# Kernel tuning notes

Hardware: AMD Instinct MI355X
Metric: run time of the kernel (lower is better)

The kernel has to match this reference:

```python
import jax, jax.numpy as jnp
import numpy as np

N_NODES = 100000
N_EDGES = 3200000
IN_CH = 128
HIDDEN = 128
N_CLASSES = 40


def setup_inputs() -> dict:
    key = jax.random.key(0)
    k1, k2, k3, k4 = jax.random.split(key, 4)
    x = jax.random.normal(k1, (N_NODES, IN_CH), dtype=jnp.float32)
    edge_index = jax.random.randint(k2, (2, N_EDGES), 0, N_NODES, dtype=jnp.int64)
    W1 = jax.random.normal(k3, (IN_CH, HIDDEN), dtype=jnp.float32) * (1.0 / np.sqrt(IN_CH))
    b1 = jnp.zeros((HIDDEN,), dtype=jnp.float32)
    W2 = jax.random.normal(k4, (HIDDEN, N_CLASSES), dtype=jnp.float32) * (1.0 / np.sqrt(HIDDEN))
    b2 = jnp.zeros((N_CLASSES,), dtype=jnp.float32)
    return {"x": x, "edge_index": edge_index, "W1": W1, "b1": b1, "W2": W2, "b2": b2}


def gcn_conv(x, src, dst, norm, W, b, n_nodes):
    # PyG GCNConv: h = x @ W; out[dst] += norm * h[src]; out += b
    h = x @ W
    msg = h[src] * norm[:, None]          # [E+N, F_out] gathered messages
    out = jax.ops.segment_sum(msg, dst, num_segments=n_nodes)
    return out + b


def reference(x, edge_index, W1, b1, W2, b2):
    n = x.shape[0]
    loop = jnp.arange(n, dtype=edge_index.dtype)
    src = jnp.concatenate([edge_index[0], loop])  # add self-loops (PyG default)
    dst = jnp.concatenate([edge_index[1], loop])
    w = jnp.ones(src.shape[0], dtype=x.dtype)
    deg = jax.ops.segment_sum(w, dst, num_segments=n)
    dinv = jnp.where(deg > 0, jax.lax.rsqrt(deg), 0.0)
    norm = dinv[src] * dinv[dst]  # symmetric normalization per edge

    h1 = jax.nn.relu(gcn_conv(x, src, dst, norm, W1, b1, n))
    # dropout is identity in eval mode
    out = gcn_conv(h1, src, dst, norm, W2, b2, n)
    return out
```

## Files before the change

kernel.cpp:

```cpp
#include <hip/hip_runtime.h>


static inline size_t align256(size_t x) { return (x + 255) & ~(size_t)255; }

#define BIN_CHUNK 16384
#define MAX_NB 511

__device__ __forceinline__ unsigned bf16pack2(float a, float b) {
  union { float f; unsigned u; } ua, ub;
  ua.f = a; ub.f = b;
  unsigned ra = (ua.u + 0x7fffu + ((ua.u >> 16) & 1u)) >> 16;
  unsigned rb = (ub.u + 0x7fffu + ((ub.u >> 16) & 1u)) >> 16;
  return ra | (rb << 16);
}

__device__ __forceinline__ void acc_bf16x8(float* acc, uint4 v) {
  union { unsigned u; float f; } c;
  c.u = v.x << 16;          acc[0] += c.f;
  c.u = v.x & 0xffff0000u;  acc[1] += c.f;
  c.u = v.y << 16;          acc[2] += c.f;
  c.u = v.y & 0xffff0000u;  acc[3] += c.f;
  c.u = v.z << 16;          acc[4] += c.f;
  c.u = v.z & 0xffff0000u;  acc[5] += c.f;
  c.u = v.w << 16;          acc[6] += c.f;
  c.u = v.w & 0xffff0000u;  acc[7] += c.f;
}

__global__ void zero_k(int* __restrict__ p, int n) {
  int i = blockIdx.x * blockDim.x + threadIdx.x;
  if (i < n) p[i] = 0;
}

__global__ __launch_bounds__(256) void bucket_count_k(const int* __restrict__ dst,
                                                      int* __restrict__ btot,
                                                      int E, int NB) {
  __shared__ int hist[MAX_NB];
  int t = threadIdx.x;
  for (int b = t; b < NB; b += 256) hist[b] = 0;
  __syncthreads();
  int e0 = blockIdx.x * BIN_CHUNK;
  int e1 = min(e0 + BIN_CHUNK, E);
  for (int e = e0 + t; e < e1; e += 256) atomicAdd(&hist[dst[e] >> 8], 1);
  __syncthreads();
  for (int b = t; b < NB; b += 256)
    if (hist[b]) atomicAdd(&btot[b], hist[b]);
}

__global__ __launch_bounds__(512) void bucket_scan_k(const int* __restrict__ btot,
                                                     int* __restrict__ base,
                                                     int* __restrict__ bcur,
                                                     int NB, int E) {
  __shared__ int ws[8];
  int t = threadIdx.x, lane = t & 63, w = t >> 6;
  int v = (t < NB) ? btot[t] : 0;
  int incl = v;
#pragma unroll
  for (int off = 1; off < 64; off <<= 1) {
    int u = __shfl_up(incl, off, 64);
    if (lane >= off) incl += u;
  }
  if (lane == 63) ws[w] = incl;
  __syncthreads();
  int woff = 0;
  for (int k = 0; k < w; ++k) woff += ws[k];
  int excl = woff + incl - v;
  if (t < NB) { base[t] = excl; bcur[t] = excl; }
  if (t == 0) base[NB] = E;
}

__global__ __launch_bounds__(256) void binpart_k(const int* __restrict__ src,
                                                 const int* __restrict__ dst,
                                                 int* __restrict__ bcur,
                                                 uint2* __restrict__ binned,
                                                 int E, int NB) {
  __shared__ int hist[MAX_NB];
  int t = threadIdx.x;
  int e0 = blockIdx.x * BIN_CHUNK;
  int e1 = min(e0 + BIN_CHUNK, E);
  for (int b = t; b < NB; b += 256) hist[b] = 0;
  __syncthreads();
  for (int e = e0 + t; e < e1; e += 256) atomicAdd(&hist[dst[e] >> 8], 1);
  __syncthreads();
  for (int b = t; b < NB; b += 256) {
    int h = hist[b];
    hist[b] = h ? atomicAdd(&bcur[b], h) : 0;
  }
  __syncthreads();
  for (int e = e0 + t; e < e1; e += 256) {
    int d = dst[e];
    int r = atomicAdd(&hist[d >> 8], 1);
    binned[r] = make_uint2((unsigned)src[e], (unsigned)d);
  }
}

__global__ __launch_bounds__(256) void binscat2_k(const uint2* __restrict__ binned,
                                                  const int* __restrict__ base,
                                                  int* __restrict__ counts,
                                                  int* __restrict__ rowoff,
                                                  float* __restrict__ dinv,
                                                  int* __restrict__ col, int N) {
  __shared__ int cnt[256];
  __shared__ int lcur[256];
  __shared__ int ws[4];
  int b = blockIdx.x, t = threadIdx.x;
  int lo = base[b], hi = base[b + 1];
  cnt[t] = 0;
  __syncthreads();
  for (int e = lo + t; e < hi; e += 256) atomicAdd(&cnt[binned[e].y & 255], 1);
  __syncthreads();
  int v = cnt[t];
  int lane = t & 63, w = t >> 6;
  int incl = v;
#pragma unroll
  for (int off = 1; off < 64; off <<= 1) {
    int u = __shfl_up(incl, off, 64);
    if (lane >= off) incl += u;
  }
  if (lane == 63) ws[w] = incl;
  __syncthreads();
  int woff = 0;
  for (int k = 0; k < w; ++k) woff += ws[k];
  int loff = woff + incl - v;
  int node = (b << 8) + t;
  if (node < N) {
    counts[node] = v;
    rowoff[node] = lo + loff;
    dinv[node] = rsqrtf((float)(v + 1));
  }
  lcur[t] = lo + loff;
  __syncthreads();
  for (int e = lo + t; e < hi; e += 256) {
    uint2 rec = binned[e];
    int p = atomicAdd(&lcur[rec.y & 255], 1);
    col[p] = (int)rec.x;
  }
}

__global__ __launch_bounds__(256) void gemm1_k(const float* __restrict__ x,
                                               const float* __restrict__ W,
                                               const float* __restrict__ dinv,
                                               unsigned* __restrict__ g1, int n) {
  __shared__ float Xs[64][68];
  __shared__ float Ws[64][132];
  int t = threadIdx.x;
  int row0 = blockIdx.x * 64;
  int cg = t & 15, rg = t >> 4;
  int c0 = cg * 8, r0 = rg * 4;

  float acc[4][8];
#pragma unroll
  for (int r = 0; r < 4; ++r)
#pragma unroll
    for (int c = 0; c < 8; ++c) acc[r][c] = 0.f;

  for (int ks = 0; ks < 2; ++ks) {
    __syncthreads();
#pragma unroll
    for (int q = 0; q < 4; ++q) {
      int f = t + q * 256;
      int r = f >> 4, c4 = f & 15;
      int grow = row0 + r;
      float4 v = make_float4(0.f, 0.f, 0.f, 0.f);
      if (grow < n) v = *(const float4*)(x + (size_t)grow * 128 + ks * 64 + c4 * 4);
      *(float4*)&Xs[r][c4 * 4] = v;
    }
#pragma unroll
    for (int q = 0; q < 8; ++q) {
      int f = t + q * 256;
      int k = f >> 5, c4 = f & 31;
      float4 v = *(const float4*)(W + (size_t)(ks * 64 + k) * 128 + c4 * 4);
      *(float4*)&Ws[k][c4 * 4] = v;
    }
    __syncthreads();

#pragma unroll
    for (int k4 = 0; k4 < 16; ++k4) {
      float4 xv0 = *(const float4*)&Xs[r0 + 0][k4 * 4];
      float4 xv1 = *(const float4*)&Xs[r0 + 1][k4 * 4];
      float4 xv2 = *(const float4*)&Xs[r0 + 2][k4 * 4];
      float4 xv3 = *(const float4*)&Xs[r0 + 3][k4 * 4];
#pragma unroll
      for (int kk = 0; kk < 4; ++kk) {
        const float* wrow = &Ws[k4 * 4 + kk][0];
        float4 wa = *(const float4*)(wrow + c0);
        float4 wb = *(const float4*)(wrow + c0 + 4);
        float a0 = kk == 0 ? xv0.x : kk == 1 ? xv0.y : kk == 2 ? xv0.z : xv0.w;
        float a1 = kk == 0 ? xv1.x : kk == 1 ? xv1.y : kk == 2 ? xv1.z : xv1.w;
        float a2 = kk == 0 ? xv2.x : kk == 1 ? xv2.y : kk == 2 ? xv2.z : xv2.w;
        float a3 = kk == 0 ? xv3.x : kk == 1 ? xv3.y : kk == 2 ? xv3.z : xv3.w;
        float as[4] = {a0, a1, a2, a3};
#pragma unroll
        for (int r = 0; r < 4; ++r) {
          acc[r][0] += as[r] * wa.x; acc[r][1] += as[r] * wa.y;
          acc[r][2] += as[r] * wa.z; acc[r][3] += as[r] * wa.w;
          acc[r][4] += as[r] * wb.x; acc[r][5] += as[r] * wb.y;
          acc[r][6] += as[r] * wb.z; acc[r][7] += as[r] * wb.w;
        }
      }
    }
  }

#pragma unroll
  for (int r = 0; r < 4; ++r) {
    int grow = row0 + r0 + r;
    if (grow < n) {
      float s = dinv[grow];
      uint4 pv;
      pv.x = bf16pack2(acc[r][0] * s, acc[r][1] * s);
      pv.y = bf16pack2(acc[r][2] * s, acc[r][3] * s);
      pv.z = bf16pack2(acc[r][4] * s, acc[r][5] * s);
      pv.w = bf16pack2(acc[r][6] * s, acc[r][7] * s);
      ((uint4*)g1)[(size_t)grow * 16 + cg] = pv;
    }
  }
}

__global__ __launch_bounds__(256) void agg1_k(const unsigned* __restrict__ g1,
                                              const int* __restrict__ col,
                                              const int* __restrict__ rowoff,
                                              const int* __restrict__ counts,
                                              const float* __restrict__ dinv,
                                              const float* __restrict__ b1,
                                              float* __restrict__ h1, int n) {
  int w = threadIdx.x >> 6, lane = threadIdx.x & 63;
  int i = blockIdx.x * 4 + w;
  if (i >= n) return;
  int q = lane >> 4, c8 = lane & 15;
  const uint4* g1v = (const uint4*)g1;
  int start = rowoff[i], cnt = counts[i];

  float acc[8] = {0.f, 0.f, 0.f, 0.f, 0.f, 0.f, 0.f, 0.f};
  if (q == 0) acc_bf16x8(acc, g1v[(size_t)i * 16 + c8]);

#pragma unroll 4
  for (int e = q; e < cnt; e += 4) {
    int j = col[start + e];
    acc_bf16x8(acc, g1v[(size_t)j * 16 + c8]);
  }

#pragma unroll
  for (int k = 0; k < 8; ++k) {
    acc[k] += __shfl_xor(acc[k], 16, 64);
    acc[k] += __shfl_xor(acc[k], 32, 64);
  }

  if (q == 0) {
    float di = dinv[i];
    float4 ba = *(const float4*)(b1 + c8 * 8);
    float4 bb = *(const float4*)(b1 + c8 * 8 + 4);
    float4 o0, o1;
    o0.x = fmaxf(di * acc[0] + ba.x, 0.f);
    o0.y = fmaxf(di * acc[1] + ba.y, 0.f);
    o0.z = fmaxf(di * acc[2] + ba.z, 0.f);
    o0.w = fmaxf(di * acc[3] + ba.w, 0.f);
    o1.x = fmaxf(di * acc[4] + bb.x, 0.f);
    o1.y = fmaxf(di * acc[5] + bb.y, 0.f);
    o1.z = fmaxf(di * acc[6] + bb.z, 0.f);
    o1.w = fmaxf(di * acc[7] + bb.w, 0.f);
    float* o = h1 + (size_t)i * 128 + c8 * 8;
    *(float4*)o = o0;
    *(float4*)(o + 4) = o1;
  }
}

__global__ __launch_bounds__(256) void gemm2_k(const float* __restrict__ h1,
                                               const float* __restrict__ W2,
                                               const float* __restrict__ dinv,
                                               unsigned* __restrict__ g2, int n) {
  __shared__ float Xs[64][68];
  __shared__ float Ws[64][68];
  int t = threadIdx.x;
  int row0 = blockIdx.x * 64;
  int cg = t & 7, rg = t >> 3;
  int c0 = cg * 8, r0 = rg * 2;

  float acc[2][8];
#pragma unroll
  for (int r = 0; r < 2; ++r)
#pragma unroll
    for (int c = 0; c < 8; ++c) acc[r][c] = 0.f;

  for (int idx = t; idx < 64 * 68; idx += 256) ((float*)Ws)[idx] = 0.f;

  for (int ks = 0; ks < 2; ++ks) {
    __syncthreads();
#pragma unroll
    for (int q = 0; q < 4; ++q) {
      int f = t + q * 256;
      int r = f >> 4, c4 = f & 15;
      int grow = row0 + r;
      float4 v = make_float4(0.f, 0.f, 0.f, 0.f);
      if (grow < n) v = *(const float4*)(h1 + (size_t)grow * 128 + ks * 64 + c4 * 4);
      *(float4*)&Xs[r][c4 * 4] = v;
    }
#pragma unroll
    for (int q = 0; q < 3; ++q) {
      int f = t + q * 256;
      if (f < 640) {
        int k = f / 10, c4 = f % 10;
        float4 v = *(const float4*)(W2 + (size_t)(ks * 64 + k) * 40 + c4 * 4);
        *(float4*)&Ws[k][c4 * 4] = v;
      }
    }
    __syncthreads();

#pragma unroll
    for (int k4 = 0; k4 < 16; ++k4) {
      float4 x0 = *(const float4*)&Xs[r0 + 0][k4 * 4];
      float4 x1 = *(const float4*)&Xs[r0 + 1][k4 * 4];
#pragma unroll
      for (int kk = 0; kk < 4; ++kk) {
        const float* wrow = &Ws[k4 * 4 + kk][0];
        float4 wa = *(const float4*)(wrow + c0);
        float4 wb = *(const float4*)(wrow + c0 + 4);
        float a0 = kk == 0 ? x0.x : kk == 1 ? x0.y : kk == 2 ? x0.z : x0.w;
        float a1 = kk == 0 ? x1.x : kk == 1 ? x1.y : kk == 2 ? x1.z : x1.w;
        acc[0][0] += a0 * wa.x; acc[0][1] += a0 * wa.y;
        acc[0][2] += a0 * wa.z; acc[0][3] += a0 * wa.w;
        acc[0][4] += a0 * wb.x; acc[0][5] += a0 * wb.y;
        acc[0][6] += a0 * wb.z; acc[0][7] += a0 * wb.w;
        acc[1][0] += a1 * wa.x; acc[1][1] += a1 * wa.y;
        acc[1][2] += a1 * wa.z; acc[1][3] += a1 * wa.w;
        acc[1][4] += a1 * wb.x; acc[1][5] += a1 * wb.y;
        acc[1][6] += a1 * wb.z; acc[1][7] += a1 * wb.w;
      }
    }
  }

#pragma unroll
  for (int r = 0; r < 2; ++r) {
    int grow = row0 + r0 + r;
    if (grow < n) {
      float s = dinv[grow];
      uint4 pv;
      pv.x = bf16pack2(acc[r][0] * s, acc[r][1] * s);
      pv.y = bf16pack2(acc[r][2] * s, acc[r][3] * s);
      pv.z = bf16pack2(acc[r][4] * s, acc[r][5] * s);
      pv.w = bf16pack2(acc[r][6] * s, acc[r][7] * s);
      ((uint4*)g2)[(size_t)grow * 8 + cg] = pv;
    }
  }
}

__global__ __launch_bounds__(256) void agg2_k(const unsigned* __restrict__ g2,
                                              const int* __restrict__ col,
                                              const int* __restrict__ rowoff,
                                              const int* __restrict__ counts,
                                              const float* __restrict__ dinv,
                                              const float* __restrict__ b2,
                                              float* __restrict__ out, int n) {
  int w = threadIdx.x >> 6, lane = threadIdx.x & 63;
  int i = blockIdx.x * 4 + w;
  if (i >= n) return;
  int q = lane >> 3, c8 = lane & 7;
  const uint4* g2v = (const uint4*)g2;
  int start = rowoff[i], cnt = counts[i];

  float acc[8] = {0.f, 0.f, 0.f, 0.f, 0.f, 0.f, 0.f, 0.f};
  if (q == 0) acc_bf16x8(acc, g2v[(size_t)i * 8 + c8]);

#pragma unroll 4
  for (int e = q; e < cnt; e += 8) {
    int j = col[start + e];
    acc_bf16x8(acc, g2v[(size_t)j * 8 + c8]);
  }

#pragma unroll
  for (int k = 0; k < 8; ++k) {
    acc[k] += __shfl_xor(acc[k], 8, 64);
    acc[k] += __shfl_xor(acc[k], 16, 64);
    acc[k] += __shfl_xor(acc[k], 32, 64);
  }

  if (lane < 5) {
    float di = dinv[i];
    float4 ba = *(const float4*)(b2 + lane * 8);
    float4 bb = *(const float4*)(b2 + lane * 8 + 4);
    float4 o0, o1;
    o0.x = di * acc[0] + ba.x;
    o0.y = di * acc[1] + ba.y;
    o0.z = di * acc[2] + ba.z;
    o0.w = di * acc[3] + ba.w;
    o1.x = di * acc[4] + bb.x;
    o1.y = di * acc[5] + bb.y;
    o1.z = di * acc[6] + bb.z;
    o1.w = di * acc[7] + bb.w;
    float* o = out + (size_t)i * 40 + lane * 8;
    *(float4*)o = o0;
    *(float4*)(o + 4) = o1;
  }
}

extern "C" void kernel_launch(void* const* d_in, const int* in_sizes, int n_in,
                              void* d_out, int out_size, void* d_ws, size_t ws_size,
                              hipStream_t stream) {
  const float* x  = (const float*)d_in[0];
  const int*   ei = (const int*)d_in[1];
  const float* W1 = (const float*)d_in[2];
  const float* b1 = (const float*)d_in[3];
  const float* W2 = (const float*)d_in[4];
  const float* b2 = (const float*)d_in[5];
  float* out = (float*)d_out;

  const int N = in_sizes[0] / 128;
  const int E = in_sizes[1] / 2;
  const int* src = ei;
  const int* dst = ei + E;
  const int NB = (N + 255) / 256;

  size_t off = 0;
  auto alloc = [&](size_t bytes) {
    char* p = (char*)d_ws + off;
    off = align256(off + bytes);
    return (void*)p;
  };
  int*      counts = (int*)alloc((size_t)N * 4);
  int*      rowoff = (int*)alloc((size_t)N * 4);
  float*    dinv   = (float*)alloc((size_t)N * 4);
  int*      btot   = (int*)alloc((size_t)NB * 4);
  int*      base   = (int*)alloc((size_t)(NB + 1) * 4);
  int*      bcur   = (int*)alloc((size_t)NB * 4);
  int*      col    = (int*)alloc((size_t)E * 4);
  uint2*    binned = (uint2*)alloc((size_t)E * 8);
  unsigned* g1     = (unsigned*)alloc((size_t)N * 128 * 2);
  float*    h1     = (float*)alloc((size_t)N * 128 * 4);
  unsigned* g2     = g1;
  if (off > ws_size) return;
  if (NB > MAX_NB) return;

  int gA = (N + 3) / 4;
  int gBin = (E + BIN_CHUNK - 1) / BIN_CHUNK;

  zero_k<<<(NB + 255) / 256, 256, 0, stream>>>(btot, NB);
  bucket_count_k<<<gBin, 256, 0, stream>>>(dst, btot, E, NB);
  bucket_scan_k<<<1, 512, 0, stream>>>(btot, base, bcur, NB, E);
  binpart_k<<<gBin, 256, 0, stream>>>(src, dst, bcur, binned, E, NB);
  binscat2_k<<<NB, 256, 0, stream>>>(binned, base, counts, rowoff, dinv, col, N);
  gemm1_k<<<(N + 63) / 64, 256, 0, stream>>>(x, W1, dinv, g1, N);
  agg1_k<<<gA, 256, 0, stream>>>(g1, col, rowoff, counts, dinv, b1, h1, N);
  gemm2_k<<<(N + 63) / 64, 256, 0, stream>>>(h1, W2, dinv, g2, N);
  agg2_k<<<gA, 256, 0, stream>>>(g2, col, rowoff, counts, dinv, b2, out, N);
}
```

Baseline: 505.7 us.

## Pack binned edge records into 32 bits and split aggregation by feature slices

The binned edge buffer now stores src<<8 | (dst&255) in one 32-bit word instead of a uint2 pair. This halves the traffic of the partition and scatter passes. The aggregation kernels now split the feature dimension into 32-channel slices handled by separate blocks. Each wave processes 16 edges in parallel per slice, with 4 lanes per 64-byte row chunk. This raises the number of edges in flight per row, but each neighbor's col index is reloaded once per slice and it adds more shuffle reductions. The src<<8 packing assumes node ids below 2^24.

```diff
diff --git a/kernel.cpp b/kernel.cpp
--- a/kernel.cpp
+++ b/kernel.cpp
@@ -71,7 +71,7 @@
 __global__ __launch_bounds__(256) void binpart_k(const int* __restrict__ src,
                                                  const int* __restrict__ dst,
                                                  int* __restrict__ bcur,
-                                                 uint2* __restrict__ binned,
+                                                 unsigned* __restrict__ binned,
                                                  int E, int NB) {
   __shared__ int hist[MAX_NB];
   int t = threadIdx.x;
@@ -89,11 +89,11 @@
   for (int e = e0 + t; e < e1; e += 256) {
     int d = dst[e];
     int r = atomicAdd(&hist[d >> 8], 1);
-    binned[r] = make_uint2((unsigned)src[e], (unsigned)d);
-  }
-}
-
-__global__ __launch_bounds__(256) void binscat2_k(const uint2* __restrict__ binned,
+    binned[r] = ((unsigned)src[e] << 8) | ((unsigned)d & 255u);
+  }
+}
+
+__global__ __launch_bounds__(256) void binscat2_k(const unsigned* __restrict__ binned,
                                                   const int* __restrict__ base,
                                                   int* __restrict__ counts,
                                                   int* __restrict__ rowoff,
@@ -106,7 +106,7 @@
   int lo = base[b], hi = base[b + 1];
   cnt[t] = 0;
   __syncthreads();
-  for (int e = lo + t; e < hi; e += 256) atomicAdd(&cnt[binned[e].y & 255], 1);
+  for (int e = lo + t; e < hi; e += 256) atomicAdd(&cnt[binned[e] & 255u], 1);
   __syncthreads();
   int v = cnt[t];
   int lane = t & 63, w = t >> 6;
@@ -130,9 +130,9 @@
   lcur[t] = lo + loff;
   __syncthreads();
   for (int e = lo + t; e < hi; e += 256) {
-    uint2 rec = binned[e];
-    int p = atomicAdd(&lcur[rec.y & 255], 1);
-    col[p] = (int)rec.x;
+    unsigned rec = binned[e];
+    int p = atomicAdd(&lcur[rec & 255u], 1);
+    col[p] = (int)(rec >> 8);
   }
 }
 
@@ -221,33 +221,39 @@
                                               const int* __restrict__ counts,
                                               const float* __restrict__ dinv,
                                               const float* __restrict__ b1,
-                                              float* __restrict__ h1, int n) {
+                                              float* __restrict__ h1, int n,
+                                              int NBA) {
   int w = threadIdx.x >> 6, lane = threadIdx.x & 63;
-  int i = blockIdx.x * 4 + w;
+  int p = blockIdx.x / NBA;
+  int i = (blockIdx.x % NBA) * 4 + w;
   if (i >= n) return;
-  int q = lane >> 4, c8 = lane & 15;
+  int q = lane >> 2, c = lane & 3;
   const uint4* g1v = (const uint4*)g1;
   int start = rowoff[i], cnt = counts[i];
+  int slice = p * 4 + c;
 
   float acc[8] = {0.f, 0.f, 0.f, 0.f, 0.f, 0.f, 0.f, 0.f};
-  if (q == 0) acc_bf16x8(acc, g1v[(size_t)i * 16 + c8]);
-
-#pragma unroll 4
-  for (int e = q; e < cnt; e += 4) {
+  if (q == 0) acc_bf16x8(acc, g1v[(size_t)i * 16 + slice]);
+
+#pragma unroll 2
+  for (int e = q; e < cnt; e += 16) {
     int j = col[start + e];
-    acc_bf16x8(acc, g1v[(size_t)j * 16 + c8]);
+    acc_bf16x8(acc, g1v[(size_t)j * 16 + slice]);
   }
 
 #pragma unroll
   for (int k = 0; k < 8; ++k) {
+    acc[k] += __shfl_xor(acc[k], 4, 64);
+    acc[k] += __shfl_xor(acc[k], 8, 64);
     acc[k] += __shfl_xor(acc[k], 16, 64);
     acc[k] += __shfl_xor(acc[k], 32, 64);
   }
 
   if (q == 0) {
     float di = dinv[i];
-    float4 ba = *(const float4*)(b1 + c8 * 8);
-    float4 bb = *(const float4*)(b1 + c8 * 8 + 4);
+    int ch = p * 32 + c * 8;
+    float4 ba = *(const float4*)(b1 + ch);
+    float4 bb = *(const float4*)(b1 + ch + 4);
     float4 o0, o1;
     o0.x = fmaxf(di * acc[0] + ba.x, 0.f);
     o0.y = fmaxf(di * acc[1] + ba.y, 0.f);
@@ -257,7 +263,7 @@
     o1.y = fmaxf(di * acc[5] + bb.y, 0.f);
     o1.z = fmaxf(di * acc[6] + bb.z, 0.f);
     o1.w = fmaxf(di * acc[7] + bb.w, 0.f);
-    float* o = h1 + (size_t)i * 128 + c8 * 8;
+    float* o = h1 + (size_t)i * 128 + ch;
     *(float4*)o = o0;
     *(float4*)(o + 4) = o1;
   }
@@ -348,34 +354,39 @@
                                               const int* __restrict__ counts,
                                               const float* __restrict__ dinv,
                                               const float* __restrict__ b2,
-                                              float* __restrict__ out, int n) {
+                                              float* __restrict__ out, int n,
+                                              int NBA) {
   int w = threadIdx.x >> 6, lane = threadIdx.x & 63;
-  int i = blockIdx.x * 4 + w;
+  int p = blockIdx.x / NBA;
+  int i = (blockIdx.x % NBA) * 4 + w;
   if (i >= n) return;
-  int q = lane >> 3, c8 = lane & 7;
+  int q = lane >> 2, c = lane & 3;
   const uint4* g2v = (const uint4*)g2;
   int start = rowoff[i], cnt = counts[i];
+  int slice = p * 4 + c;
 
   float acc[8] = {0.f, 0.f, 0.f, 0.f, 0.f, 0.f, 0.f, 0.f};
-  if (q == 0) acc_bf16x8(acc, g2v[(size_t)i * 8 + c8]);
-
-#pragma unroll 4
-  for (int e = q; e < cnt; e += 8) {
+  if (q == 0) acc_bf16x8(acc, g2v[(size_t)i * 8 + slice]);
+
+#pragma unroll 2
+  for (int e = q; e < cnt; e += 16) {
     int j = col[start + e];
-    acc_bf16x8(acc, g2v[(size_t)j * 8 + c8]);
+    acc_bf16x8(acc, g2v[(size_t)j * 8 + slice]);
   }
 
 #pragma unroll
   for (int k = 0; k < 8; ++k) {
+    acc[k] += __shfl_xor(acc[k], 4, 64);
     acc[k] += __shfl_xor(acc[k], 8, 64);
     acc[k] += __shfl_xor(acc[k], 16, 64);
     acc[k] += __shfl_xor(acc[k], 32, 64);
   }
 
-  if (lane < 5) {
+  int ch = p * 32 + c * 8;
+  if (q == 0 && ch < 40) {
     float di = dinv[i];
-    float4 ba = *(const float4*)(b2 + lane * 8);
-    float4 bb = *(const float4*)(b2 + lane * 8 + 4);
+    float4 ba = *(const float4*)(b2 + ch);
+    float4 bb = *(const float4*)(b2 + ch + 4);
     float4 o0, o1;
     o0.x = di * acc[0] + ba.x;
     o0.y = di * acc[1] + ba.y;
@@ -385,7 +396,7 @@
     o1.y = di * acc[5] + bb.y;
     o1.z = di * acc[6] + bb.z;
     o1.w = di * acc[7] + bb.w;
-    float* o = out + (size_t)i * 40 + lane * 8;
+    float* o = out + (size_t)i * 40 + ch;
     *(float4*)o = o0;
     *(float4*)(o + 4) = o1;
   }
@@ -421,14 +432,14 @@
   int*      base   = (int*)alloc((size_t)(NB + 1) * 4);
   int*      bcur   = (int*)alloc((size_t)NB * 4);
   int*      col    = (int*)alloc((size_t)E * 4);
-  uint2*    binned = (uint2*)alloc((size_t)E * 8);
+  unsigned* binned = (unsigned*)alloc((size_t)E * 4);
   unsigned* g1     = (unsigned*)alloc((size_t)N * 128 * 2);
   float*    h1     = (float*)alloc((size_t)N * 128 * 4);
   unsigned* g2     = g1;
   if (off > ws_size) return;
   if (NB > MAX_NB) return;
 
-  int gA = (N + 3) / 4;
+  const int NBA = (N + 3) / 4;
   int gBin = (E + BIN_CHUNK - 1) / BIN_CHUNK;
 
   zero_k<<<(NB + 255) / 256, 256, 0, stream>>>(btot, NB);
@@ -437,7 +448,7 @@
   binpart_k<<<gBin, 256, 0, stream>>>(src, dst, bcur, binned, E, NB);
   binscat2_k<<<NB, 256, 0, stream>>>(binned, base, counts, rowoff, dinv, col, N);
   gemm1_k<<<(N + 63) / 64, 256, 0, stream>>>(x, W1, dinv, g1, N);
-  agg1_k<<<gA, 256, 0, stream>>>(g1, col, rowoff, counts, dinv, b1, h1, N);
+  agg1_k<<<4 * NBA, 256, 0, stream>>>(g1, col, rowoff, counts, dinv, b1, h1, N, NBA);
   gemm2_k<<<(N + 63) / 64, 256, 0, stream>>>(h1, W2, dinv, g2, N);
-  agg2_k<<<gA, 256, 0, stream>>>(g2, col, rowoff, counts, dinv, b2, out, N);
-}
+  agg2_k<<<2 * NBA, 256, 0, stream>>>(g2, col, rowoff, counts, dinv, b2, out, N, NBA);
+}
```

Measured after the change: 620.6 us. +22.7%, slower.

## Use bf16 MFMA for first GEMM and pack binned edges into 32 bits

Applied to the files above, without the earlier changes.

The first-layer GEMM moves from scalar fp32 FMAs to bf16 MFMA 16x16x32 instructions. It uses a 128-row tile, converts inputs to bf16 in LDS, and stages the output through LDS for coalesced stores. Separately, each binned edge record is packed into one 32-bit word (src<<8 | dst&255) instead of a uint2, which halves the traffic of the binning pass. The bf16 rounding of x and W1 adds precision loss, and the packing assumes src fits in 24 bits.

```diff
diff --git a/kernel.cpp b/kernel.cpp
--- a/kernel.cpp
+++ b/kernel.cpp
@@ -5,6 +5,9 @@
 
 #define BIN_CHUNK 16384
 #define MAX_NB 511
+
+typedef float f32x4 __attribute__((ext_vector_type(4)));
+typedef short s16x8 __attribute__((ext_vector_type(8)));
 
 __device__ __forceinline__ unsigned bf16pack2(float a, float b) {
   union { float f; unsigned u; } ua, ub;
@@ -71,7 +74,7 @@
 __global__ __launch_bounds__(256) void binpart_k(const int* __restrict__ src,
                                                  const int* __restrict__ dst,
                                                  int* __restrict__ bcur,
-                                                 uint2* __restrict__ binned,
+                                                 unsigned* __restrict__ binned,
                                                  int E, int NB) {
   __shared__ int hist[MAX_NB];
   int t = threadIdx.x;
@@ -89,11 +92,11 @@
   for (int e = e0 + t; e < e1; e += 256) {
     int d = dst[e];
     int r = atomicAdd(&hist[d >> 8], 1);
-    binned[r] = make_uint2((unsigned)src[e], (unsigned)d);
-  }
-}
-
-__global__ __launch_bounds__(256) void binscat2_k(const uint2* __restrict__ binned,
+    binned[r] = ((unsigned)src[e] << 8) | ((unsigned)d & 255u);
+  }
+}
+
+__global__ __launch_bounds__(256) void binscat2_k(const unsigned* __restrict__ binned,
                                                   const int* __restrict__ base,
                                                   int* __restrict__ counts,
                                                   int* __restrict__ rowoff,
@@ -106,7 +109,7 @@
   int lo = base[b], hi = base[b + 1];
   cnt[t] = 0;
   __syncthreads();
-  for (int e = lo + t; e < hi; e += 256) atomicAdd(&cnt[binned[e].y & 255], 1);
+  for (int e = lo + t; e < hi; e += 256) atomicAdd(&cnt[binned[e] & 255u], 1);
   __syncthreads();
   int v = cnt[t];
   int lane = t & 63, w = t >> 6;
@@ -130,87 +133,116 @@
   lcur[t] = lo + loff;
   __syncthreads();
   for (int e = lo + t; e < hi; e += 256) {
-    uint2 rec = binned[e];
-    int p = atomicAdd(&lcur[rec.y & 255], 1);
-    col[p] = (int)rec.x;
-  }
-}
-
+    unsigned rec = binned[e];
+    int p = atomicAdd(&lcur[rec & 255u], 1);
+    col[p] = (int)(rec >> 8);
+  }
+}
+
+#define AP 72
+#define CPI 136
 __global__ __launch_bounds__(256) void gemm1_k(const float* __restrict__ x,
                                                const float* __restrict__ W,
                                                const float* __restrict__ dinv,
                                                unsigned* __restrict__ g1, int n) {
-  __shared__ float Xs[64][68];
-  __shared__ float Ws[64][132];
+  __shared__ short lds[2][128 * AP];
+  __shared__ float dinv_s[128];
+  short* As = &lds[0][0];
+  short* Bs = &lds[1][0];
   int t = threadIdx.x;
-  int row0 = blockIdx.x * 64;
-  int cg = t & 15, rg = t >> 4;
-  int c0 = cg * 8, r0 = rg * 4;
-
-  float acc[4][8];
-#pragma unroll
-  for (int r = 0; r < 4; ++r)
-#pragma unroll
-    for (int c = 0; c < 8; ++c) acc[r][c] = 0.f;
+  int row0 = blockIdx.x * 128;
+  int lane = t & 63, wv = t >> 6;
+  int R = (wv >> 1) * 64, C = (wv & 1) * 64;
+  int m16 = lane & 15, quad = lane >> 4;
+
+  if (t < 128) {
+    int grow = row0 + t;
+    dinv_s[t] = (grow < n) ? dinv[grow] : 0.f;
+  }
+
+  f32x4 acc[4][4] = {};
 
   for (int ks = 0; ks < 2; ++ks) {
     __syncthreads();
-#pragma unroll
-    for (int q = 0; q < 4; ++q) {
-      int f = t + q * 256;
-      int r = f >> 4, c4 = f & 15;
+    {
+      int r = t >> 1, h = t & 1;
       int grow = row0 + r;
-      float4 v = make_float4(0.f, 0.f, 0.f, 0.f);
-      if (grow < n) v = *(const float4*)(x + (size_t)grow * 128 + ks * 64 + c4 * 4);
-      *(float4*)&Xs[r][c4 * 4] = v;
-    }
-#pragma unroll
-    for (int q = 0; q < 8; ++q) {
-      int f = t + q * 256;
-      int k = f >> 5, c4 = f & 31;
-      float4 v = *(const float4*)(W + (size_t)(ks * 64 + k) * 128 + c4 * 4);
-      *(float4*)&Ws[k][c4 * 4] = v;
-    }
-    __syncthreads();
-
-#pragma unroll
-    for (int k4 = 0; k4 < 16; ++k4) {
-      float4 xv0 = *(const float4*)&Xs[r0 + 0][k4 * 4];
-      float4 xv1 = *(const float4*)&Xs[r0 + 1][k4 * 4];
-      float4 xv2 = *(const float4*)&Xs[r0 + 2][k4 * 4];
-      float4 xv3 = *(const float4*)&Xs[r0 + 3][k4 * 4];
-#pragma unroll
-      for (int kk = 0; kk < 4; ++kk) {
-        const float* wrow = &Ws[k4 * 4 + kk][0];
-        float4 wa = *(const float4*)(wrow + c0);
-        float4 wb = *(const float4*)(wrow + c0 + 4);
-        float a0 = kk == 0 ? xv0.x : kk == 1 ? xv0.y : kk == 2 ? xv0.z : xv0.w;
-        float a1 = kk == 0 ? xv1.x : kk == 1 ? xv1.y : kk == 2 ? xv1.z : xv1.w;
-        float a2 = kk == 0 ? xv2.x : kk == 1 ? xv2.y : kk == 2 ? xv2.z : xv2.w;
-        float a3 = kk == 0 ? xv3.x : kk == 1 ? xv3.y : kk == 2 ? xv3.z : xv3.w;
-        float as[4] = {a0, a1, a2, a3};
-#pragma unroll
-        for (int r = 0; r < 4; ++r) {
-          acc[r][0] += as[r] * wa.x; acc[r][1] += as[r] * wa.y;
-          acc[r][2] += as[r] * wa.z; acc[r][3] += as[r] * wa.w;
-          acc[r][4] += as[r] * wb.x; acc[r][5] += as[r] * wb.y;
-          acc[r][6] += as[r] * wb.z; acc[r][7] += as[r] * wb.w;
+      const float* xr = x + (size_t)grow * 128 + ks * 64 + h * 32;
+      short* dp = As + r * AP + h * 32;
+      if (grow < n) {
+#pragma unroll
+        for (int kk = 0; kk < 8; ++kk) {
+          float4 v = *(const float4*)(xr + kk * 4);
+          *(unsigned*)(dp + kk * 4)     = bf16pack2(v.x, v.y);
+          *(unsigned*)(dp + kk * 4 + 2) = bf16pack2(v.z, v.w);
+        }
+      } else {
+#pragma unroll
+        for (int kk = 0; kk < 8; ++kk) {
+          *(unsigned*)(dp + kk * 4)     = 0u;
+          *(unsigned*)(dp + kk * 4 + 2) = 0u;
         }
       }
     }
-  }
-
-#pragma unroll
-  for (int r = 0; r < 4; ++r) {
-    int grow = row0 + r0 + r;
+    {
+      int ng = t & 31, kp8 = t >> 5;
+      int n4 = ng * 4;
+#pragma unroll
+      for (int kk = 0; kk < 4; ++kk) {
+        int kp = kp8 + kk * 8;
+        int k = ks * 64 + kp * 2;
+        float4 w0 = *(const float4*)(W + (size_t)k * 128 + n4);
+        float4 w1 = *(const float4*)(W + (size_t)(k + 1) * 128 + n4);
+        *(unsigned*)&Bs[(n4 + 0) * AP + kp * 2] = bf16pack2(w0.x, w1.x);
+        *(unsigned*)&Bs[(n4 + 1) * AP + kp * 2] = bf16pack2(w0.y, w1.y);
+        *(unsigned*)&Bs[(n4 + 2) * AP + kp * 2] = bf16pack2(w0.z, w1.z);
+        *(unsigned*)&Bs[(n4 + 3) * AP + kp * 2] = bf16pack2(w0.w, w1.w);
+      }
+    }
+    __syncthreads();
+
+#pragma unroll
+    for (int kq = 0; kq < 2; ++kq) {
+      int k0 = kq * 32 + quad * 8;
+      s16x8 a[4], b[4];
+#pragma unroll
+      for (int i = 0; i < 4; ++i)
+        a[i] = *(const s16x8*)&As[(R + i * 16 + m16) * AP + k0];
+#pragma unroll
+      for (int j = 0; j < 4; ++j)
+        b[j] = *(const s16x8*)&Bs[(C + j * 16 + m16) * AP + k0];
+#pragma unroll
+      for (int i = 0; i < 4; ++i)
+#pragma unroll
+        for (int j = 0; j < 4; ++j)
+          acc[i][j] = __builtin_amdgcn_mfma_f32_16x16x32_bf16(a[i], b[j], acc[i][j], 0, 0, 0);
+    }
+  }
+
+  __syncthreads();
+  short* Cs = &lds[0][0];
+#pragma unroll
+  for (int i = 0; i < 4; ++i) {
+#pragma unroll
+    for (int reg = 0; reg < 4; ++reg) {
+      int rl = R + i * 16 + quad * 4 + reg;
+      float di = dinv_s[rl];
+#pragma unroll
+      for (int j = 0; j < 4; ++j) {
+        float val = acc[i][j][reg] * di;
+        Cs[rl * CPI + C + j * 16 + m16] = (short)(bf16pack2(val, 0.f) & 0xffffu);
+      }
+    }
+  }
+  __syncthreads();
+#pragma unroll
+  for (int it = 0; it < 8; ++it) {
+    int idx = t + it * 256;
+    int r = idx >> 4, u = idx & 15;
+    int grow = row0 + r;
     if (grow < n) {
-      float s = dinv[grow];
-      uint4 pv;
-      pv.x = bf16pack2(acc[r][0] * s, acc[r][1] * s);
-      pv.y = bf16pack2(acc[r][2] * s, acc[r][3] * s);
-      pv.z = bf16pack2(acc[r][4] * s, acc[r][5] * s);
-      pv.w = bf16pack2(acc[r][6] * s, acc[r][7] * s);
-      ((uint4*)g1)[(size_t)grow * 16 + cg] = pv;
+      uint4 v = *(const uint4*)&Cs[r * CPI + u * 8];
+      ((uint4*)g1)[(size_t)grow * 16 + u] = v;
     }
   }
 }
@@ -421,7 +453,7 @@
   int*      base   = (int*)alloc((size_t)(NB + 1) * 4);
   int*      bcur   = (int*)alloc((size_t)NB * 4);
   int*      col    = (int*)alloc((size_t)E * 4);
-  uint2*    binned = (uint2*)alloc((size_t)E * 8);
+  unsigned* binned = (unsigned*)alloc((size_t)E * 4);
   unsigned* g1     = (unsigned*)alloc((size_t)N * 128 * 2);
   float*    h1     = (float*)alloc((size_t)N * 128 * 4);
   unsigned* g2     = g1;
@@ -436,7 +468,7 @@
   bucket_scan_k<<<1, 512, 0, stream>>>(btot, base, bcur, NB, E);
   binpart_k<<<gBin, 256, 0, stream>>>(src, dst, bcur, binned, E, NB);
   binscat2_k<<<NB, 256, 0, stream>>>(binned, base, counts, rowoff, dinv, col, N);
-  gemm1_k<<<(N + 63) / 64, 256, 0, stream>>>(x, W1, dinv, g1, N);
+  gemm1_k<<<(N + 127) / 128, 256, 0, stream>>>(x, W1, dinv, g1, N);
   agg1_k<<<gA, 256, 0, stream>>>(g1, col, rowoff, counts, dinv, b1, h1, N);
   gemm2_k<<<(N + 63) / 64, 256, 0, stream>>>(h1, W2, dinv, g2, N);
   agg2_k<<<gA, 256, 0, stream>>>(g2, col, rowoff, counts, dinv, b2, out, N);
```

After: 455.1 us. 10.0% less time.
